# Optimization experiments

Hardware: AMD Instinct MI355X
Metric: run time of the kernel (lower is better)

The kernel has to match this reference:

```python
import jax, jax.numpy as jnp
import numpy as np

S, I, H, FC, O = 16384, 64, 1024, 128, 1


def setup_inputs() -> dict:
    key = jax.random.key(0)
    ks = jax.random.split(key, 9)
    s_lstm = 1.0 / np.sqrt(H)
    return {
        "input_seq": jax.random.normal(ks[0], (S, I), jnp.float32),
        "W_ih": jax.random.uniform(ks[1], (4 * H, I), jnp.float32, -s_lstm, s_lstm),
        "W_hh": jax.random.uniform(ks[2], (4 * H, H), jnp.float32, -s_lstm, s_lstm),
        "b_ih": jax.random.uniform(ks[3], (4 * H,), jnp.float32, -s_lstm, s_lstm),
        "b_hh": jax.random.uniform(ks[4], (4 * H,), jnp.float32, -s_lstm, s_lstm),
        "fc1_w": jax.random.uniform(ks[5], (FC, H), jnp.float32, -s_lstm, s_lstm),
        "fc1_b": jax.random.uniform(ks[6], (FC,), jnp.float32, -s_lstm, s_lstm),
        "fc2_w": jax.random.uniform(ks[7], (O, FC), jnp.float32, -1.0 / np.sqrt(FC), 1.0 / np.sqrt(FC)),
        "fc2_b": jax.random.uniform(ks[8], (O,), jnp.float32, -1.0 / np.sqrt(FC), 1.0 / np.sqrt(FC)),
    }


def _lstm_scan(x, W_ih, W_hh, b_ih, b_hh):
    # PyTorch gate order: i, f, g, o. batch=1 collapsed; x: [S, I]
    xg = x @ W_ih.T + (b_ih + b_hh)  # precompute input-side gates: [S, 4H]

    def step(carry, xg_t):
        h, c = carry
        gates = xg_t + h @ W_hh.T
        i, f, g, o = jnp.split(gates, 4)
        i = jax.nn.sigmoid(i)
        f = jax.nn.sigmoid(f)
        g = jnp.tanh(g)
        o = jax.nn.sigmoid(o)
        c = f * c + i * g
        h = o * jnp.tanh(c)
        return (h, c), h

    h0 = jnp.zeros((H,), x.dtype)
    c0 = jnp.zeros((H,), x.dtype)
    _, hs = jax.lax.scan(step, (h0, c0), xg)
    return hs  # [S, H]


def reference(input_seq, W_ih, W_hh, b_ih, b_hh, fc1_w, fc1_b, fc2_w, fc2_b):
    hs = _lstm_scan(input_seq, W_ih, W_hh, b_ih, b_hh)       # [S, H]
    x = jax.nn.relu(hs)                                       # relu on LSTM outputs
    x = jax.nn.relu(x @ fc1_w.T + fc1_b)                      # [S, 128]
    x = x @ fc2_w.T + fc2_b                                   # [S, 1]
    return x[-1]                                              # [1]
```

## Files before the change

kernel.cpp:

```cpp
#include <hip/hip_runtime.h>
#include <hip/hip_fp16.h>


#define S_LEN 16384
#define I_DIM 64
#define H_DIM 1024
#define NBLK  64
#define NTHR  1024

__device__ __forceinline__ float sigmoidf_(float x) { return 1.0f / (1.0f + __expf(-x)); }
__device__ __forceinline__ float tanh_fast(float x) { return 1.0f - 2.0f / (__expf(2.0f * x) + 1.0f); }

__device__ __forceinline__ unsigned pack_pair(unsigned tag, float h) {
    return (tag << 16) | (unsigned)__half_as_ushort(__float2half(h));
}
__device__ __forceinline__ float unpack_val(unsigned pk) {
    return __half2float(__ushort_as_half((unsigned short)(pk & 0xFFFFu)));
}

__global__ __launch_bounds__(NTHR, 4) void lstm_persistent(
    const float* __restrict__ xseq,
    const float* __restrict__ W_ih,
    const float* __restrict__ W_hh,
    const float* __restrict__ b_ih,
    const float* __restrict__ b_hh,
    unsigned* __restrict__ pairs)
{
    const int b   = blockIdx.x;
    const int tid = threadIdx.x;
    const int w   = tid >> 6;
    const int c   = tid & 63;
    const int g   = w >> 2;
    const int r0  = (w & 3) * 4;

    __shared__ float4 h_stage[H_DIM / 4];
    __shared__ float  x_stage[2][I_DIM];
    __shared__ float  gs[64];
    __shared__ float  bias_s[64];

    float4 wh[4][4];
    float  wi[4];
    #pragma unroll
    for (int q = 0; q < 4; ++q) {
        const int grow = g * H_DIM + 16 * b + r0 + q;
        const float4* wr = (const float4*)(W_hh + (size_t)grow * H_DIM);
        #pragma unroll
        for (int s = 0; s < 4; ++s) wh[q][s] = wr[s * 64 + c];
        wi[q] = W_ih[(size_t)grow * I_DIM + c];
    }
    if (tid < 64) {
        const int grow = (tid >> 4) * H_DIM + 16 * b + (tid & 15);
        bias_s[tid] = b_ih[grow] + b_hh[grow];
    }
    float cst = 0.0f;
    if (tid < H_DIM / 4) h_stage[tid] = make_float4(0.f, 0.f, 0.f, 0.f);
    if (tid < 16) ((float4*)x_stage[0])[tid] = ((const float4*)xseq)[tid];
    const bool own = (tid >> 4) == b;
    __syncthreads();

    for (int t = 0; t < S_LEN; ++t) {
        if (tid < 16 && t + 1 < S_LEN)
            ((float4*)x_stage[(t + 1) & 1])[tid] =
                ((const float4*)(xseq + (size_t)(t + 1) * I_DIM))[tid];

        float acc[4] = {0.f, 0.f, 0.f, 0.f};
        #pragma unroll
        for (int s = 0; s < 4; ++s) {
            const float4 hv = h_stage[s * 64 + c];
            #pragma unroll
            for (int q = 0; q < 4; ++q) {
                acc[q] = fmaf(wh[q][s].x, hv.x, acc[q]);
                acc[q] = fmaf(wh[q][s].y, hv.y, acc[q]);
                acc[q] = fmaf(wh[q][s].z, hv.z, acc[q]);
                acc[q] = fmaf(wh[q][s].w, hv.w, acc[q]);
            }
        }
        {
            const float xv = x_stage[t & 1][c];
            #pragma unroll
            for (int q = 0; q < 4; ++q) acc[q] = fmaf(wi[q], xv, acc[q]);
        }
        #pragma unroll
        for (int q = 0; q < 4; ++q) {
            #pragma unroll
            for (int off = 32; off > 0; off >>= 1)
                acc[q] += __shfl_xor(acc[q], off, 64);
        }
        if (c == 0) {
            #pragma unroll
            for (int q = 0; q < 4; ++q) gs[g * 16 + r0 + q] = acc[q];
        }
        __syncthreads();

        if (tid < 16) {
            const float pi  = gs[tid]      + bias_s[tid];
            const float pfg = gs[16 + tid] + bias_s[16 + tid];
            const float pg  = gs[32 + tid] + bias_s[32 + tid];
            const float po  = gs[48 + tid] + bias_s[48 + tid];
            const float ig = sigmoidf_(pi);
            const float fg = sigmoidf_(pfg);
            const float gg = tanh_fast(pg);
            const float og = sigmoidf_(po);
            cst = fg * cst + ig * gg;
            const float h = og * tanh_fast(cst);
            const unsigned pk = pack_pair((unsigned)(t + 1), h);
            __hip_atomic_store(&pairs[(size_t)(t & 1) * H_DIM + 16 * b + tid], pk,
                               __ATOMIC_RELAXED, __HIP_MEMORY_SCOPE_AGENT);
            ((float*)h_stage)[16 * b + tid] = unpack_val(pk);
        }

        if (t == S_LEN - 1) break;

        if (!own) {
            const unsigned tag = (unsigned)(t + 1);
            const unsigned* p = &pairs[(size_t)(t & 1) * H_DIM + tid];
            unsigned pk;
            for (;;) {
                pk = __hip_atomic_load(p, __ATOMIC_RELAXED, __HIP_MEMORY_SCOPE_AGENT);
                if ((pk >> 16) == tag) break;
                __builtin_amdgcn_s_sleep(1);
            }
            ((float*)h_stage)[tid] = unpack_val(pk);
        }
        __syncthreads();
    }
}

__global__ __launch_bounds__(256) void fc_head(
    const unsigned* __restrict__ pairs,
    const float* __restrict__ fc1_w,
    const float* __restrict__ fc1_b,
    const float* __restrict__ fc2_w,
    const float* __restrict__ fc2_b,
    float* __restrict__ out)
{
    const int tid = threadIdx.x;
    __shared__ float4 hr4[H_DIM / 4];
    __shared__ float  partial[256];
    __shared__ float  r1[128];

    const uint4 pa = ((const uint4*)(pairs + H_DIM))[tid];
    float4 hv = make_float4(__half2float(__ushort_as_half((unsigned short)(pa.x & 0xFFFFu))),
                            __half2float(__ushort_as_half((unsigned short)(pa.y & 0xFFFFu))),
                            __half2float(__ushort_as_half((unsigned short)(pa.z & 0xFFFFu))),
                            __half2float(__ushort_as_half((unsigned short)(pa.w & 0xFFFFu))));
    hv.x = fmaxf(hv.x, 0.f); hv.y = fmaxf(hv.y, 0.f);
    hv.z = fmaxf(hv.z, 0.f); hv.w = fmaxf(hv.w, 0.f);
    hr4[tid] = hv;
    __syncthreads();

    const int row = tid & 127, half = tid >> 7;
    const float4* wrow = (const float4*)(fc1_w + (size_t)row * H_DIM) + half * 128;
    float a0 = 0.f, a1 = 0.f;
    #pragma unroll 4
    for (int i = 0; i < 128; i += 2) {
        const float4 w0 = wrow[i],     h0 = hr4[half * 128 + i];
        const float4 w1 = wrow[i + 1], h1 = hr4[half * 128 + i + 1];
        a0 += w0.x * h0.x + w0.y * h0.y + w0.z * h0.z + w0.w * h0.w;
        a1 += w1.x * h1.x + w1.y * h1.y + w1.z * h1.z + w1.w * h1.w;
    }
    partial[tid] = a0 + a1;
    __syncthreads();
    if (tid < 128) {
        const float s = partial[tid] + partial[tid + 128] + fc1_b[tid];
        r1[tid] = fmaxf(s, 0.f);
    }
    __syncthreads();
    if (tid < 64) {
        float v = r1[tid] * fc2_w[tid] + r1[tid + 64] * fc2_w[tid + 64];
        #pragma unroll
        for (int off = 32; off > 0; off >>= 1) v += __shfl_xor(v, off, 64);
        if (tid == 0) out[0] = v + fc2_b[0];
    }
}

extern "C" void kernel_launch(void* const* d_in, const int* in_sizes, int n_in,
                              void* d_out, int out_size, void* d_ws, size_t ws_size,
                              hipStream_t stream) {
    (void)in_sizes; (void)n_in; (void)out_size; (void)ws_size;
    const float* xseq  = (const float*)d_in[0];
    const float* W_ih  = (const float*)d_in[1];
    const float* W_hh  = (const float*)d_in[2];
    const float* b_ih  = (const float*)d_in[3];
    const float* b_hh  = (const float*)d_in[4];
    const float* fc1_w = (const float*)d_in[5];
    const float* fc1_b = (const float*)d_in[6];
    const float* fc2_w = (const float*)d_in[7];
    const float* fc2_b = (const float*)d_in[8];
    unsigned* pairs = (unsigned*)d_ws;

    lstm_persistent<<<NBLK, NTHR, 0, stream>>>(xseq, W_ih, W_hh, b_ih, b_hh, pairs);
    fc_head<<<1, 256, 0, stream>>>(pairs, fc1_w, fc1_b, fc2_w, fc2_b, (float*)d_out);
}
```

Before: 40.51 ms.

## Replace 64-block persistent LSTM with 512 single-wave blocks polling global state

Restructures the persistent LSTM from 64 blocks of 1024 threads, which used shared-memory staging and __syncthreads, into 512 single-wavefront blocks that each own two hidden columns. Every wave holds 128 W_hh weights per lane in registers and polls the whole packed fp16/tag h vector straight from global memory, with 16 loads per lane and a wave-wide __all check. This removes the intra-block barriers and the LDS round trips. In exchange, global polling traffic grows a lot (512 waves each reading all 1024 entries every step), register pressure rises, and correctness depends on all 512 blocks being co-resident.

After: 70.65 ms. 1.74x slower.

```diff
diff --git a/kernel.cpp b/kernel.cpp
--- a/kernel.cpp
+++ b/kernel.cpp
@@ -5,20 +5,12 @@
 #define S_LEN 16384
 #define I_DIM 64
 #define H_DIM 1024
-#define NBLK  64
-#define NTHR  1024
+#define NWAVE 512
 
 __device__ __forceinline__ float sigmoidf_(float x) { return 1.0f / (1.0f + __expf(-x)); }
 __device__ __forceinline__ float tanh_fast(float x) { return 1.0f - 2.0f / (__expf(2.0f * x) + 1.0f); }
 
-__device__ __forceinline__ unsigned pack_pair(unsigned tag, float h) {
-    return (tag << 16) | (unsigned)__half_as_ushort(__float2half(h));
-}
-__device__ __forceinline__ float unpack_val(unsigned pk) {
-    return __half2float(__ushort_as_half((unsigned short)(pk & 0xFFFFu)));
-}
-
-__global__ __launch_bounds__(NTHR, 4) void lstm_persistent(
+__global__ __launch_bounds__(64, 1) void lstm_wave(
     const float* __restrict__ xseq,
     const float* __restrict__ W_ih,
     const float* __restrict__ W_hh,
@@ -26,103 +18,97 @@
     const float* __restrict__ b_hh,
     unsigned* __restrict__ pairs)
 {
-    const int b   = blockIdx.x;
-    const int tid = threadIdx.x;
-    const int w   = tid >> 6;
-    const int c   = tid & 63;
-    const int g   = w >> 2;
-    const int r0  = (w & 3) * 4;
+    const int wv   = blockIdx.x;
+    const int c    = threadIdx.x;
+    const int col0 = 2 * wv;
 
-    __shared__ float4 h_stage[H_DIM / 4];
-    __shared__ float  x_stage[2][I_DIM];
-    __shared__ float  gs[64];
-    __shared__ float  bias_s[64];
+    float wh[8][16];
+    float wi[8];
+    #pragma unroll
+    for (int r = 0; r < 8; ++r) {
+        const int q = r >> 1, j = r & 1;
+        const size_t row = (size_t)q * H_DIM + col0 + j;
+        const float* wr = W_hh + row * H_DIM;
+        #pragma unroll
+        for (int s = 0; s < 4; ++s)
+            #pragma unroll
+            for (int u = 0; u < 4; ++u)
+                wh[r][s * 4 + u] = wr[s * 256 + u * 64 + c];
+        wi[r] = W_ih[row * I_DIM + c];
+    }
+    float bsum[4];
+    {
+        const int mycol = col0 + (c & 1);
+        #pragma unroll
+        for (int q = 0; q < 4; ++q)
+            bsum[q] = b_ih[q * H_DIM + mycol] + b_hh[q * H_DIM + mycol];
+    }
 
-    float4 wh[4][4];
-    float  wi[4];
-    #pragma unroll
-    for (int q = 0; q < 4; ++q) {
-        const int grow = g * H_DIM + 16 * b + r0 + q;
-        const float4* wr = (const float4*)(W_hh + (size_t)grow * H_DIM);
-        #pragma unroll
-        for (int s = 0; s < 4; ++s) wh[q][s] = wr[s * 64 + c];
-        wi[q] = W_ih[(size_t)grow * I_DIM + c];
-    }
-    if (tid < 64) {
-        const int grow = (tid >> 4) * H_DIM + 16 * b + (tid & 15);
-        bias_s[tid] = b_ih[grow] + b_hh[grow];
-    }
     float cst = 0.0f;
-    if (tid < H_DIM / 4) h_stage[tid] = make_float4(0.f, 0.f, 0.f, 0.f);
-    if (tid < 16) ((float4*)x_stage[0])[tid] = ((const float4*)xseq)[tid];
-    const bool own = (tid >> 4) == b;
-    __syncthreads();
+    float xv  = xseq[c];
+    unsigned pk[4][4];
 
     for (int t = 0; t < S_LEN; ++t) {
-        if (tid < 16 && t + 1 < S_LEN)
-            ((float4*)x_stage[(t + 1) & 1])[tid] =
-                ((const float4*)(xseq + (size_t)(t + 1) * I_DIM))[tid];
+        float acc[8];
+        #pragma unroll
+        for (int r = 0; r < 8; ++r) acc[r] = wi[r] * xv;
 
-        float acc[4] = {0.f, 0.f, 0.f, 0.f};
-        #pragma unroll
-        for (int s = 0; s < 4; ++s) {
-            const float4 hv = h_stage[s * 64 + c];
+        if (t > 0) {
             #pragma unroll
-            for (int q = 0; q < 4; ++q) {
-                acc[q] = fmaf(wh[q][s].x, hv.x, acc[q]);
-                acc[q] = fmaf(wh[q][s].y, hv.y, acc[q]);
-                acc[q] = fmaf(wh[q][s].z, hv.z, acc[q]);
-                acc[q] = fmaf(wh[q][s].w, hv.w, acc[q]);
+            for (int s = 0; s < 4; ++s) {
+                #pragma unroll
+                for (int u = 0; u < 4; ++u) {
+                    const float hv = __half2float(
+                        __ushort_as_half((unsigned short)(pk[s][u] & 0xFFFFu)));
+                    #pragma unroll
+                    for (int r = 0; r < 8; ++r)
+                        acc[r] = fmaf(wh[r][s * 4 + u], hv, acc[r]);
+                }
             }
         }
-        {
-            const float xv = x_stage[t & 1][c];
-            #pragma unroll
-            for (int q = 0; q < 4; ++q) acc[q] = fmaf(wi[q], xv, acc[q]);
-        }
+
         #pragma unroll
-        for (int q = 0; q < 4; ++q) {
+        for (int r = 0; r < 8; ++r) {
             #pragma unroll
             for (int off = 32; off > 0; off >>= 1)
-                acc[q] += __shfl_xor(acc[q], off, 64);
+                acc[r] += __shfl_xor(acc[r], off, 64);
         }
-        if (c == 0) {
-            #pragma unroll
-            for (int q = 0; q < 4; ++q) gs[g * 16 + r0 + q] = acc[q];
-        }
-        __syncthreads();
 
-        if (tid < 16) {
-            const float pi  = gs[tid]      + bias_s[tid];
-            const float pfg = gs[16 + tid] + bias_s[16 + tid];
-            const float pg  = gs[32 + tid] + bias_s[32 + tid];
-            const float po  = gs[48 + tid] + bias_s[48 + tid];
-            const float ig = sigmoidf_(pi);
-            const float fg = sigmoidf_(pfg);
-            const float gg = tanh_fast(pg);
-            const float og = sigmoidf_(po);
+        if (c < 2) {
+            const float a_i = (c & 1) ? acc[1] : acc[0];
+            const float a_f = (c & 1) ? acc[3] : acc[2];
+            const float a_g = (c & 1) ? acc[5] : acc[4];
+            const float a_o = (c & 1) ? acc[7] : acc[6];
+            const float ig = sigmoidf_(a_i + bsum[0]);
+            const float fg = sigmoidf_(a_f + bsum[1]);
+            const float gg = tanh_fast (a_g + bsum[2]);
+            const float og = sigmoidf_(a_o + bsum[3]);
             cst = fg * cst + ig * gg;
             const float h = og * tanh_fast(cst);
-            const unsigned pk = pack_pair((unsigned)(t + 1), h);
-            __hip_atomic_store(&pairs[(size_t)(t & 1) * H_DIM + 16 * b + tid], pk,
+            const unsigned pkv = ((unsigned)(t + 1) << 16) |
+                                 (unsigned)__half_as_ushort(__float2half(h));
+            __hip_atomic_store(&pairs[((size_t)(t & 1) << 10) + col0 + c], pkv,
                                __ATOMIC_RELAXED, __HIP_MEMORY_SCOPE_AGENT);
-            ((float*)h_stage)[16 * b + tid] = unpack_val(pk);
         }
 
         if (t == S_LEN - 1) break;
 
-        if (!own) {
-            const unsigned tag = (unsigned)(t + 1);
-            const unsigned* p = &pairs[(size_t)(t & 1) * H_DIM + tid];
-            unsigned pk;
-            for (;;) {
-                pk = __hip_atomic_load(p, __ATOMIC_RELAXED, __HIP_MEMORY_SCOPE_AGENT);
-                if ((pk >> 16) == tag) break;
-                __builtin_amdgcn_s_sleep(1);
-            }
-            ((float*)h_stage)[tid] = unpack_val(pk);
+        xv = xseq[(size_t)(t + 1) * I_DIM + c];
+
+        const unsigned* base = pairs + ((size_t)(t & 1) << 10) + c;
+        const unsigned tgs = (unsigned)(t + 1) << 16;
+        for (;;) {
+            unsigned bad = 0;
+            #pragma unroll
+            for (int s = 0; s < 4; ++s)
+                #pragma unroll
+                for (int u = 0; u < 4; ++u) {
+                    pk[s][u] = __hip_atomic_load(base + s * 256 + u * 64,
+                                                 __ATOMIC_RELAXED, __HIP_MEMORY_SCOPE_AGENT);
+                    bad |= pk[s][u] ^ tgs;
+                }
+            if (__all((bad >> 16) == 0)) break;
         }
-        __syncthreads();
     }
 }
 
@@ -189,6 +175,6 @@
     const float* fc2_b = (const float*)d_in[8];
     unsigned* pairs = (unsigned*)d_ws;
 
-    lstm_persistent<<<NBLK, NTHR, 0, stream>>>(xseq, W_ih, W_hh, b_ih, b_hh, pairs);
+    lstm_wave<<<NWAVE, 64, 0, stream>>>(xseq, W_ih, W_hh, b_ih, b_hh, pairs);
     fc_head<<<1, 256, 0, stream>>>(pairs, fc1_w, fc1_b, fc2_w, fc2_b, (float*)d_out);
 }
```

## Remap waves to hidden columns, double-buffer h, pipeline spin-wait loads

Applied to the files above, without the earlier changes.

Each wave now owns one hidden unit and holds all four of its gate rows, so the gate nonlinearities and cell update run right after the wave shuffle reduction. This removes the shared gs staging and one __syncthreads per timestep. The h staging buffer is double-buffered so a single barrier per step is enough. The x input is read straight from global memory into a register, and the spin-wait keeps three atomic loads in flight with no sleep, trading extra memory polling for lower wake-up latency.

Result: slower. 74.34 ms (+83.5%).

```diff
diff --git a/kernel.cpp b/kernel.cpp
--- a/kernel.cpp
+++ b/kernel.cpp
@@ -10,10 +10,6 @@
 
 __device__ __forceinline__ float sigmoidf_(float x) { return 1.0f / (1.0f + __expf(-x)); }
 __device__ __forceinline__ float tanh_fast(float x) { return 1.0f - 2.0f / (__expf(2.0f * x) + 1.0f); }
-
-__device__ __forceinline__ unsigned pack_pair(unsigned tag, float h) {
-    return (tag << 16) | (unsigned)__half_as_ushort(__float2half(h));
-}
 __device__ __forceinline__ float unpack_val(unsigned pk) {
     return __half2float(__ushort_as_half((unsigned short)(pk & 0xFFFFu)));
 }
@@ -30,97 +26,85 @@
     const int tid = threadIdx.x;
     const int w   = tid >> 6;
     const int c   = tid & 63;
-    const int g   = w >> 2;
-    const int r0  = (w & 3) * 4;
+    const int col = 16 * b + w;
 
-    __shared__ float4 h_stage[H_DIM / 4];
-    __shared__ float  x_stage[2][I_DIM];
-    __shared__ float  gs[64];
-    __shared__ float  bias_s[64];
+    __shared__ float4 h_stage[2][H_DIM / 4];
 
     float4 wh[4][4];
     float  wi[4];
+    float  bsum[4];
     #pragma unroll
     for (int q = 0; q < 4; ++q) {
-        const int grow = g * H_DIM + 16 * b + r0 + q;
-        const float4* wr = (const float4*)(W_hh + (size_t)grow * H_DIM);
+        const size_t row = (size_t)q * H_DIM + col;
+        const float4* wr = (const float4*)(W_hh + row * H_DIM);
         #pragma unroll
-        for (int s = 0; s < 4; ++s) wh[q][s] = wr[s * 64 + c];
-        wi[q] = W_ih[(size_t)grow * I_DIM + c];
+        for (int m = 0; m < 4; ++m) wh[q][m] = wr[m * 64 + c];
+        wi[q]   = W_ih[row * I_DIM + c];
+        bsum[q] = b_ih[row] + b_hh[row];
     }
-    if (tid < 64) {
-        const int grow = (tid >> 4) * H_DIM + 16 * b + (tid & 15);
-        bias_s[tid] = b_ih[grow] + b_hh[grow];
-    }
+
+    if (tid < H_DIM / 4) h_stage[0][tid] = make_float4(0.f, 0.f, 0.f, 0.f);
+    const bool own = (tid >> 4) == b;
     float cst = 0.0f;
-    if (tid < H_DIM / 4) h_stage[tid] = make_float4(0.f, 0.f, 0.f, 0.f);
-    if (tid < 16) ((float4*)x_stage[0])[tid] = ((const float4*)xseq)[tid];
-    const bool own = (tid >> 4) == b;
+    float xv  = xseq[c];
     __syncthreads();
 
     for (int t = 0; t < S_LEN; ++t) {
-        if (tid < 16 && t + 1 < S_LEN)
-            ((float4*)x_stage[(t + 1) & 1])[tid] =
-                ((const float4*)(xseq + (size_t)(t + 1) * I_DIM))[tid];
+        const int cur = t & 1, nxt = cur ^ 1;
 
-        float acc[4] = {0.f, 0.f, 0.f, 0.f};
+        float acc0 = wi[0] * xv, acc1 = wi[1] * xv, acc2 = wi[2] * xv, acc3 = wi[3] * xv;
         #pragma unroll
-        for (int s = 0; s < 4; ++s) {
-            const float4 hv = h_stage[s * 64 + c];
-            #pragma unroll
-            for (int q = 0; q < 4; ++q) {
-                acc[q] = fmaf(wh[q][s].x, hv.x, acc[q]);
-                acc[q] = fmaf(wh[q][s].y, hv.y, acc[q]);
-                acc[q] = fmaf(wh[q][s].z, hv.z, acc[q]);
-                acc[q] = fmaf(wh[q][s].w, hv.w, acc[q]);
-            }
+        for (int m = 0; m < 4; ++m) {
+            const float4 hv = h_stage[cur][m * 64 + c];
+            acc0 = fmaf(wh[0][m].x, hv.x, acc0); acc0 = fmaf(wh[0][m].y, hv.y, acc0);
+            acc0 = fmaf(wh[0][m].z, hv.z, acc0); acc0 = fmaf(wh[0][m].w, hv.w, acc0);
+            acc1 = fmaf(wh[1][m].x, hv.x, acc1); acc1 = fmaf(wh[1][m].y, hv.y, acc1);
+            acc1 = fmaf(wh[1][m].z, hv.z, acc1); acc1 = fmaf(wh[1][m].w, hv.w, acc1);
+            acc2 = fmaf(wh[2][m].x, hv.x, acc2); acc2 = fmaf(wh[2][m].y, hv.y, acc2);
+            acc2 = fmaf(wh[2][m].z, hv.z, acc2); acc2 = fmaf(wh[2][m].w, hv.w, acc2);
+            acc3 = fmaf(wh[3][m].x, hv.x, acc3); acc3 = fmaf(wh[3][m].y, hv.y, acc3);
+            acc3 = fmaf(wh[3][m].z, hv.z, acc3); acc3 = fmaf(wh[3][m].w, hv.w, acc3);
         }
-        {
-            const float xv = x_stage[t & 1][c];
-            #pragma unroll
-            for (int q = 0; q < 4; ++q) acc[q] = fmaf(wi[q], xv, acc[q]);
+
+        if (t + 1 < S_LEN) xv = xseq[(size_t)(t + 1) * I_DIM + c];
+
+        #pragma unroll
+        for (int off = 32; off > 0; off >>= 1) {
+            acc0 += __shfl_xor(acc0, off, 64);
+            acc1 += __shfl_xor(acc1, off, 64);
+            acc2 += __shfl_xor(acc2, off, 64);
+            acc3 += __shfl_xor(acc3, off, 64);
         }
-        #pragma unroll
-        for (int q = 0; q < 4; ++q) {
-            #pragma unroll
-            for (int off = 32; off > 0; off >>= 1)
-                acc[q] += __shfl_xor(acc[q], off, 64);
-        }
+
+        const float ig = sigmoidf_(acc0 + bsum[0]);
+        const float fg = sigmoidf_(acc1 + bsum[1]);
+        const float gg = tanh_fast (acc2 + bsum[2]);
+        const float og = sigmoidf_(acc3 + bsum[3]);
+        cst = fg * cst + ig * gg;
+        const float h = og * tanh_fast(cst);
+        const unsigned pkv = ((unsigned)(t + 1) << 16) |
+                             (unsigned)__half_as_ushort(__float2half(h));
         if (c == 0) {
-            #pragma unroll
-            for (int q = 0; q < 4; ++q) gs[g * 16 + r0 + q] = acc[q];
-        }
-        __syncthreads();
-
-        if (tid < 16) {
-            const float pi  = gs[tid]      + bias_s[tid];
-            const float pfg = gs[16 + tid] + bias_s[16 + tid];
-            const float pg  = gs[32 + tid] + bias_s[32 + tid];
-            const float po  = gs[48 + tid] + bias_s[48 + tid];
-            const float ig = sigmoidf_(pi);
-            const float fg = sigmoidf_(pfg);
-            const float gg = tanh_fast(pg);
-            const float og = sigmoidf_(po);
-            cst = fg * cst + ig * gg;
-            const float h = og * tanh_fast(cst);
-            const unsigned pk = pack_pair((unsigned)(t + 1), h);
-            __hip_atomic_store(&pairs[(size_t)(t & 1) * H_DIM + 16 * b + tid], pk,
+            __hip_atomic_store(&pairs[(size_t)cur * H_DIM + col], pkv,
                                __ATOMIC_RELAXED, __HIP_MEMORY_SCOPE_AGENT);
-            ((float*)h_stage)[16 * b + tid] = unpack_val(pk);
+            ((float*)h_stage[nxt])[col] = unpack_val(pkv);
         }
 
         if (t == S_LEN - 1) break;
 
         if (!own) {
             const unsigned tag = (unsigned)(t + 1);
-            const unsigned* p = &pairs[(size_t)(t & 1) * H_DIM + tid];
+            const unsigned* p = &pairs[(size_t)cur * H_DIM + tid];
+            unsigned a0 = __hip_atomic_load(p, __ATOMIC_RELAXED, __HIP_MEMORY_SCOPE_AGENT);
+            unsigned a1 = __hip_atomic_load(p, __ATOMIC_RELAXED, __HIP_MEMORY_SCOPE_AGENT);
+            unsigned a2 = __hip_atomic_load(p, __ATOMIC_RELAXED, __HIP_MEMORY_SCOPE_AGENT);
             unsigned pk;
             for (;;) {
-                pk = __hip_atomic_load(p, __ATOMIC_RELAXED, __HIP_MEMORY_SCOPE_AGENT);
-                if ((pk >> 16) == tag) break;
-                __builtin_amdgcn_s_sleep(1);
+                if ((a0 >> 16) == tag) { pk = a0; break; }
+                a0 = a1; a1 = a2;
+                a2 = __hip_atomic_load(p, __ATOMIC_RELAXED, __HIP_MEMORY_SCOPE_AGENT);
             }
-            ((float*)h_stage)[tid] = unpack_val(pk);
+            ((float*)h_stage[nxt])[tid] = unpack_val(pk);
         }
         __syncthreads();
     }
```
